# Performance work log

Measured on AMD Instinct MI355X. Metric: run time of the kernel, lower is better.

## Reference

```python
import jax, jax.numpy as jnp
import numpy as np

GRID_DIMS = (64, 64, 64)
GRID_LOWER = np.array([0.0, 0.0, 0.0], np.float32)
GRID_STEPS = np.array([0.015625, 0.015625, 0.015625], np.float32)
RADIUS = 0.03125
STENCIL = 2  # ceil(radius / step)


def _poly6(d2, h):
    # standard SPH poly6 smoothing kernel: 315/(64 pi h^9) (h^2 - d^2)^3, d <= h
    c = np.float32(315.0 / (64.0 * np.pi * h ** 9))
    return jnp.where(d2 <= h * h, c * (h * h - d2) ** 3, 0.0)


def particles2grid(locs, data, density):
    # locs [B,N,3], data [B,N,C], density [B,N] -> grid [B,X,Y,Z,C]
    B, N, _ = locs.shape
    C = data.shape[-1]
    X, Y, Z = GRID_DIMS
    dims = jnp.array(GRID_DIMS, jnp.int32)
    r = jnp.arange(-STENCIL, STENCIL + 1)
    offs = jnp.stack(jnp.meshgrid(r, r, r, indexing='ij'), -1).reshape(-1, 3)  # [K,3]
    base = jnp.floor((locs - GRID_LOWER) / GRID_STEPS).astype(jnp.int32)        # [B,N,3]
    cells = base[:, :, None, :] + offs                                          # [B,N,K,3]
    centers = GRID_LOWER + (cells.astype(locs.dtype) + 0.5) * GRID_STEPS
    d2 = jnp.sum((centers - locs[:, :, None, :]) ** 2, -1)                      # [B,N,K]
    w = _poly6(d2, RADIUS)
    w = jnp.where(jnp.all((cells >= 0) & (cells < dims), -1), w, 0.0)
    contrib = w[..., None] * (data / density[..., None])[:, :, None, :]         # [B,N,K,C]
    cells = jnp.clip(cells, 0, dims - 1)
    flat = (cells[..., 0] * Y + cells[..., 1]) * Z + cells[..., 2]              # [B,N,K]

    def splat(f, c):
        return jnp.zeros((X * Y * Z, C), data.dtype).at[f.reshape(-1)].add(c.reshape(-1, C))

    return jax.vmap(splat)(flat, contrib).reshape(B, X, Y, Z, C)


def grid2particles(grid, locs):
    # trilinear interpolation of grid [B,X,Y,Z,C] at particle locations [B,N,3]
    B, X, Y, Z, C = grid.shape
    dims = jnp.array([X, Y, Z], jnp.int32)
    pos = (locs - GRID_LOWER) / GRID_STEPS - 0.5                                # cell-center coords
    i0 = jnp.floor(pos).astype(jnp.int32)
    frac = pos - i0.astype(locs.dtype)
    gflat = grid.reshape(B, X * Y * Z, C)
    gather = jax.vmap(lambda g, f: g[f])                                        # [B,N] -> [B,N,C]
    out = jnp.zeros((B, locs.shape[1], C), grid.dtype)
    for dx in (0, 1):
        for dy in (0, 1):
            for dz in (0, 1):
                off = jnp.array([dx, dy, dz], jnp.int32)
                idx = i0 + off
                wd = jnp.where(off == 1, frac, 1.0 - frac)                      # [B,N,3]
                w = wd[..., 0] * wd[..., 1] * wd[..., 2]
                w = jnp.where(jnp.all((idx >= 0) & (idx < dims), -1), w, 0.0)
                idx = jnp.clip(idx, 0, dims - 1)
                flat = (idx[..., 0] * Y + idx[..., 1]) * Z + idx[..., 2]
                out = out + w[..., None] * gather(gflat, flat)
    return out


def conv3d(x, w, b):
    y = jax.lax.conv_general_dilated(x, w, (1, 1, 1), 'SAME',
                                     dimension_numbers=('NCDHW', 'OIDHW', 'NCDHW'))
    return y + b[None, :, None, None, None]


def prelu(x, a):
    return jnp.where(x >= 0, x, a * x)


def setup_inputs() -> dict:
    key = jax.random.key(0)
    ks = jax.random.split(key, 8)
    B, N = 2, 32768
    Cin, K, Cout = 4, 32, 4
    s = lambda fan: np.float32(1.0 / np.sqrt(fan * 27))
    return {
        'locs': jax.random.uniform(ks[0], (B, N, 3), jnp.float32),
        'data': jax.random.normal(ks[1], (B, N, Cin), jnp.float32),
        'density': jax.random.uniform(ks[2], (B, N), jnp.float32, 0.5, 1.5),
        'W0': jax.random.normal(ks[3], (K, Cin, 3, 3, 3), jnp.float32) * s(Cin),
        'b0': jnp.zeros((K,), jnp.float32),
        'W1': jax.random.normal(ks[4], (K, K, 3, 3, 3), jnp.float32) * s(K),
        'b1': jnp.zeros((K,), jnp.float32),
        'W2': jax.random.normal(ks[5], (K, K, 3, 3, 3), jnp.float32) * s(K),
        'b2': jnp.zeros((K,), jnp.float32),
        'W3': jax.random.normal(ks[6], (Cout, K, 3, 3, 3), jnp.float32) * s(K),
        'b3': jnp.zeros((Cout,), jnp.float32),
        'a0': jnp.full((1,), 0.25, jnp.float32),
        'a1': jnp.full((1,), 0.25, jnp.float32),
        'a2': jnp.full((1,), 0.25, jnp.float32),
    }


def reference(locs, data, density, W0, b0, W1, b1, W2, b2, W3, b3, a0, a1, a2):
    grid = particles2grid(locs, data, density)            # [B,X,Y,Z,Cin]
    g = jnp.transpose(grid, (0, 4, 1, 2, 3))              # NCDHW
    g = prelu(conv3d(g, W0, b0), a0)
    g = prelu(conv3d(g, W1, b1), a1)
    g = prelu(conv3d(g, W2, b2), a2)
    g = conv3d(g, W3, b3)
    g = jnp.transpose(g, (0, 2, 3, 4, 1))                 # [B,X,Y,Z,Cout]
    return grid2particles(g, locs)                        # [B,N,Cout]
```

## Files before the change

kernel.cpp:

```cpp
#include <hip/hip_runtime.h>

#define BATCH 2
#define NPART 32768
#define GD 64
#define NVOX (BATCH * GD * GD * GD)

typedef unsigned short ushortT;
typedef __attribute__((ext_vector_type(8))) short short8;
typedef __attribute__((ext_vector_type(16))) float float16;

__device__ __forceinline__ float poly6_c() {
    const double H9 = 1.0 / 35184372088832.0;
    return (float)(315.0 / (64.0 * 3.14159265358979323846 * H9));
}

__device__ __forceinline__ ushortT bf16_rne(float f) {
    unsigned int u = __float_as_uint(f);
    u = (u + 0x7fffu + ((u >> 16) & 1u)) >> 16;
    return (ushortT)u;
}

__device__ __forceinline__ int imax(int a, int b) { return a > b ? a : b; }
__device__ __forceinline__ int imin(int a, int b) { return a < b ? a : b; }

__device__ __forceinline__ void load_lds16(const void* g, void* l) {
    __builtin_amdgcn_global_load_lds(
        (const __attribute__((address_space(1))) void*)g,
        (__attribute__((address_space(3))) void*)l, 16, 0, 0);
}

__global__ void zero_ints_kernel(int* __restrict__ p, int n) {
    int t = blockIdx.x * blockDim.x + threadIdx.x;
    if (t < n) p[t] = 0;
}

__global__ __launch_bounds__(256) void bin_count_kernel(
    const float* __restrict__ locs, int* __restrict__ counts) {
    int t = blockIdx.x * blockDim.x + threadIdx.x;
    if (t >= BATCH * NPART) return;
    int b = t >> 15;
    int bx = ((int)floorf(locs[t * 3 + 0] * 64.0f)) >> 1;
    int by = ((int)floorf(locs[t * 3 + 1] * 64.0f)) >> 1;
    int bz = ((int)floorf(locs[t * 3 + 2] * 64.0f)) >> 1;
    atomicAdd(&counts[b * 32768 + ((bx * 32) + by) * 32 + bz], 1);
}

__global__ __launch_bounds__(256) void scanA_kernel(
    const int* __restrict__ counts, int* __restrict__ offsets,
    int* __restrict__ blockSum) {
    __shared__ int sh[256];
    int tid = threadIdx.x, g = blockIdx.x;
    int v = counts[g * 256 + tid];
    sh[tid] = v;
    __syncthreads();
    for (int off = 1; off < 256; off <<= 1) {
        int u = (tid >= off) ? sh[tid - off] : 0;
        __syncthreads();
        sh[tid] += u;
        __syncthreads();
    }
    offsets[g * 256 + tid] = sh[tid] - v;
    if (tid == 255) blockSum[g] = sh[255];
}

__global__ __launch_bounds__(256) void scanB_kernel(
    int* __restrict__ offsets, const int* __restrict__ blockSum) {
    __shared__ int sh[256];
    int tid = threadIdx.x, g = blockIdx.x;
    sh[tid] = (tid < g) ? blockSum[tid] : 0;
    __syncthreads();
    for (int off = 128; off > 0; off >>= 1) {
        if (tid < off) sh[tid] += sh[tid + off];
        __syncthreads();
    }
    offsets[g * 256 + tid] += sh[0];
    if (g == 255 && tid == 255) offsets[65536] = BATCH * NPART;
}

__global__ __launch_bounds__(256) void bin_scatter_kernel(
    const float* __restrict__ locs, const float* __restrict__ data,
    const float* __restrict__ density, const int* __restrict__ offsets,
    int* __restrict__ cursor, float* __restrict__ payload) {
    int t = blockIdx.x * blockDim.x + threadIdx.x;
    if (t >= BATCH * NPART) return;
    int b = t >> 15;
    float px = locs[t * 3 + 0];
    float py = locs[t * 3 + 1];
    float pz = locs[t * 3 + 2];
    int bx = ((int)floorf(px * 64.0f)) >> 1;
    int by = ((int)floorf(py * 64.0f)) >> 1;
    int bz = ((int)floorf(pz * 64.0f)) >> 1;
    int bb = b * 32768 + ((bx * 32) + by) * 32 + bz;
    int slot = atomicAdd(&cursor[bb], 1);
    int idx = offsets[bb] + slot;
    float inv_d = 1.0f / density[t];
    float4 p0 = {px, py, pz, data[t * 4 + 0] * inv_d};
    float4 p1 = {data[t * 4 + 1] * inv_d, data[t * 4 + 2] * inv_d,
                 data[t * 4 + 3] * inv_d, 0.f};
    *(float4*)(payload + idx * 8)     = p0;
    *(float4*)(payload + idx * 8 + 4) = p1;
}

__global__ __launch_bounds__(256) void splat_gather_kernel(
    const float* __restrict__ payload, const int* __restrict__ offsets,
    ushortT* __restrict__ g8) {
    __shared__ float plist[256 * 8];
    __shared__ int segS[36];
    __shared__ int segP[37];
    __shared__ int shTot[1];

    int wg = blockIdx.x;
    int sb = wg & 511, b = wg >> 9;
    int X0 = (sb >> 6) * 8, Y0 = ((sb >> 3) & 7) * 8, Z0 = (sb & 7) * 8;
    int tid = threadIdx.x;

    int bxlo = imax(0, (X0 - 2) >> 1), bxhi = imin(31, (X0 + 9) >> 1);
    int bylo = imax(0, (Y0 - 2) >> 1), byhi = imin(31, (Y0 + 9) >> 1);
    int bzlo = imax(0, (Z0 - 2) >> 1), bzhi = imin(31, (Z0 + 9) >> 1);
    int ny = byhi - bylo + 1;
    int ns = (bxhi - bxlo + 1) * ny;
    if (tid < ns) {
        int bx = bxlo + tid / ny, by = bylo + tid % ny;
        int row = b * 32768 + (bx * 32 + by) * 32;
        int s = offsets[row + bzlo];
        int e = offsets[row + bzhi + 1];
        segS[tid] = s;
        segP[tid] = e - s;
    }
    __syncthreads();
    if (tid == 0) {
        int p = 0;
        for (int k = 0; k < ns; ++k) { int len = segP[k]; segP[k] = p; p += len; }
        segP[ns] = p;
        shTot[0] = p;
    }
    __syncthreads();

    const float step = 0.015625f;
    const float h2 = 0.03125f * 0.03125f;
    const float cc = poly6_c();
    int total = shTot[0];

    int l = tid & 63, w = tid >> 6;
    int cx = X0 + 4 * (w >> 1) + (l >> 4);
    int cy = Y0 + 4 * (w & 1) + ((l >> 2) & 3);
    int cz0 = Z0 + (l & 3);
    float xc  = ((float)cx  + 0.5f) * step;
    float yc  = ((float)cy  + 0.5f) * step;
    float zc0 = ((float)cz0 + 0.5f) * step;
    float zc1 = zc0 + 4.0f * step;

    float a00 = 0.f, a01 = 0.f, a02 = 0.f, a03 = 0.f;
    float a10 = 0.f, a11 = 0.f, a12 = 0.f, a13 = 0.f;

    int nchunks = (total + 255) >> 8;
    for (int ch = 0; ch < nchunks; ++ch) {
        __syncthreads();
        int jj = (ch << 8) + tid;
        if (jj < total) {
            int k = 0;
            while (jj >= segP[k + 1]) ++k;
            int idx = segS[k] + (jj - segP[k]);
            *(float4*)(plist + tid * 8)     = *(const float4*)(payload + idx * 8);
            *(float4*)(plist + tid * 8 + 4) = *(const float4*)(payload + idx * 8 + 4);
        }
        __syncthreads();
        int cnt = imin(256, total - (ch << 8));
        for (int p = 0; p < cnt; ++p) {
            float4 pa = *(const float4*)(plist + p * 8);
            float dx = pa.x - xc, dy = pa.y - yc;
            float dxy2 = fmaf(dy, dy, dx * dx);
            if (!__any(dxy2 <= h2)) continue;
            float4 pv = *(const float4*)(plist + p * 8 + 4);
            float dz0 = pa.z - zc0;
            float d20 = fmaf(dz0, dz0, dxy2);
            float u0 = fmaxf(h2 - d20, 0.f);
            float w0 = (cc * u0) * (u0 * u0);
            a00 = fmaf(w0, pa.w, a00);
            a01 = fmaf(w0, pv.x, a01);
            a02 = fmaf(w0, pv.y, a02);
            a03 = fmaf(w0, pv.z, a03);
            float dz1 = pa.z - zc1;
            float d21 = fmaf(dz1, dz1, dxy2);
            float u1 = fmaxf(h2 - d21, 0.f);
            float w1 = (cc * u1) * (u1 * u1);
            a10 = fmaf(w1, pa.w, a10);
            a11 = fmaf(w1, pv.x, a11);
            a12 = fmaf(w1, pv.y, a12);
            a13 = fmaf(w1, pv.z, a13);
        }
    }

    size_t cellBase = (size_t)(((b * 64 + cx) * 64 + cy) * 64);
    short8 o;
    o[0] = (short)bf16_rne(a00); o[1] = (short)bf16_rne(a01);
    o[2] = (short)bf16_rne(a02); o[3] = (short)bf16_rne(a03);
    o[4] = 0; o[5] = 0; o[6] = 0; o[7] = 0;
    *(short8*)(g8 + (cellBase + cz0) * 8) = o;
    o[0] = (short)bf16_rne(a10); o[1] = (short)bf16_rne(a11);
    o[2] = (short)bf16_rne(a12); o[3] = (short)bf16_rne(a13);
    *(short8*)(g8 + (cellBase + cz0 + 4) * 8) = o;
}

__global__ void repack_all_kernel(
    const float* __restrict__ W0, const float* __restrict__ W1,
    const float* __restrict__ W2, const float* __restrict__ W3,
    short* __restrict__ Bp) {
    int t = blockIdx.x * blockDim.x + threadIdx.x;
    if (t >= 176 * 512) return;
    int kt = t >> 9;
    const float* W; int O, I, CINP, ktL;
    if (kt < 14)       { W = W0; O = 32; I = 4;  CINP = 8;  ktL = kt; }
    else if (kt < 68)  { W = W1; O = 32; I = 32; CINP = 32; ktL = kt - 14; }
    else if (kt < 122) { W = W2; O = 32; I = 32; CINP = 32; ktL = kt - 68; }
    else               { W = W3; O = 4;  I = 32; CINP = 32; ktL = kt - 122; }
    int l = (t >> 3) & 63, j = t & 7;
    int n = l & 31, q = l >> 5;
    int k = ktL * 16 + 8 * q + j;
    int tap = k / CINP;
    int ic  = k - tap * CINP;
    float v = 0.f;
    if (tap < 27 && ic < I && n < O) v = W[(n * I + ic) * 27 + tap];
    Bp[t] = (short)bf16_rne(v);
}

template <int ICG, int KT, bool FINAL>
__global__ __launch_bounds__(256, 3) void mfma_conv_kernel(
    const ushortT* __restrict__ in, const short* __restrict__ Bpack,
    const float* __restrict__ bias, const float* __restrict__ alpha,
    const float* __restrict__ zguard, void* __restrict__ outv) {
    constexpr int CIN = ICG * 8;
    constexpr int NCH = 24 * ICG * 34;
    __shared__ short lds[NCH * 8];
    int wg = ((blockIdx.x & 7) << 8) | (blockIdx.x >> 3);
    int zh = wg & 1, yq = (wg >> 1) & 15, xp = (wg >> 5) & 31, b = wg >> 10;
    int X0 = xp * 2, Y0 = yq * 4, Z0 = zh * 32;
    int tid = threadIdx.x;

    const ushortT* inb = in + (size_t)b * (64 * 64 * 64 * CIN);
#pragma unroll
    for (int it = 0; it < (NCH + 255) / 256; ++it) {
        int ccid = it * 256 + tid;
        if (ccid < NCH) {
            int col = ccid / (ICG * 34);
            int rem = ccid - col * (ICG * 34);
            int icg = rem / 34;
            int zi  = rem - icg * 34;
            int gx = X0 + col / 6 - 1;
            int gy = Y0 + col % 6 - 1;
            int gz = Z0 + zi - 1;
            const void* src = (const void*)zguard;
            if ((unsigned)gx < 64u && (unsigned)gy < 64u && (unsigned)gz < 64u)
                src = (const void*)(inb + ((size_t)(((gx * 64) + gy) * 64 + gz)) * CIN + icg * 8);
            load_lds16(src, (void*)(lds + ccid * 8));
        }
    }
    __syncthreads();

    int l = tid & 63, w = tid >> 6;
    int wx = w >> 1;
    int cyA = (w & 1) * 2, cyB = cyA + 1;
    int n = l & 31, q = l >> 5;

    float bval = FINAL ? (n < 4 ? bias[n] : 0.f) : bias[n];
    float16 accA, accB;
#pragma unroll
    for (int r = 0; r < 16; ++r) { accA[r] = bval; accB[r] = bval; }

    const short* bp = Bpack + (size_t)l * 8;
    int laneZ = (l & 31) * 8;

    short8 bf[4];
#pragma unroll
    for (int i = 0; i < 4; ++i) bf[i] = *(const short8*)(bp + i * 512);

#pragma unroll
    for (int kt = 0; kt < KT; ++kt) {
        short8 bcur = bf[kt & 3];
        if (kt + 4 < KT) bf[kt & 3] = *(const short8*)(bp + (kt + 4) * 512);
        int aofsA, aofsB;
        if constexpr (ICG == 1) {
            int tap0 = kt * 2, tap1 = kt * 2 + 1;
            if (tap1 > 26) tap1 = 26;
            int dx0 = tap0 / 9, r0 = tap0 - dx0 * 9, dy0 = r0 / 3, dz0 = r0 - dy0 * 3;
            int dx1 = tap1 / 9, r1 = tap1 - dx1 * 9, dy1 = r1 / 3, dz1 = r1 - dy1 * 3;
            int cA0 = (((wx + dx0) * 6 + (cyA + dy0)) * 34 + dz0) * 8;
            int cA1 = (((wx + dx1) * 6 + (cyA + dy1)) * 34 + dz1) * 8;
            int cB0 = (((wx + dx0) * 6 + (cyB + dy0)) * 34 + dz0) * 8;
            int cB1 = (((wx + dx1) * 6 + (cyB + dy1)) * 34 + dz1) * 8;
            aofsA = q ? cA1 : cA0;
            aofsB = q ? cB1 : cB0;
        } else {
            int tap = kt >> 1;
            int dx = tap / 9, rr = tap - dx * 9, dy = rr / 3, dz = rr - dy * 3;
            int icg = (kt & 1) * 2 + q;
            aofsA = ((((wx + dx) * 6 + (cyA + dy)) * ICG + icg) * 34 + dz) * 8;
            aofsB = ((((wx + dx) * 6 + (cyB + dy)) * ICG + icg) * 34 + dz) * 8;
        }
        short8 afragA = *(const short8*)(lds + aofsA + laneZ);
        short8 afragB = *(const short8*)(lds + aofsB + laneZ);
        accA = __builtin_amdgcn_mfma_f32_32x32x16_bf16(afragA, bcur, accA, 0, 0, 0);
        accB = __builtin_amdgcn_mfma_f32_32x32x16_bf16(afragB, bcur, accB, 0, 0, 0);
    }

    size_t baseA = (size_t)(((b * 64 + X0 + wx) * 64 + (Y0 + cyA)) * 64) + Z0;
    size_t baseB = (size_t)(((b * 64 + X0 + wx) * 64 + (Y0 + cyB)) * 64) + Z0;
    if (FINAL) {
        float* out = (float*)outv;
        if (n < 4) {
#pragma unroll
            for (int r = 0; r < 16; ++r) {
                int z = (r & 3) + 8 * (r >> 2) + 4 * q;
                out[(baseA + z) * 4 + n] = accA[r];
                out[(baseB + z) * 4 + n] = accB[r];
            }
        }
    } else {
        float a = alpha[0];
        ushortT* out = (ushortT*)outv;
#pragma unroll
        for (int r = 0; r < 16; ++r) {
            int z = (r & 3) + 8 * (r >> 2) + 4 * q;
            float vA = accA[r];
            vA = vA >= 0.f ? vA : a * vA;
            out[(baseA + z) * 32 + n] = bf16_rne(vA);
            float vB = accB[r];
            vB = vB >= 0.f ? vB : a * vB;
            out[(baseB + z) * 32 + n] = bf16_rne(vB);
        }
    }
}

__global__ __launch_bounds__(256) void gather_kernel(
    const float* __restrict__ grid, const float* __restrict__ locs,
    float* __restrict__ out) {
    int t = blockIdx.x * blockDim.x + threadIdx.x;
    if (t >= BATCH * NPART) return;
    int b = t >> 15;

    float px = locs[t * 3 + 0] * 64.0f - 0.5f;
    float py = locs[t * 3 + 1] * 64.0f - 0.5f;
    float pz = locs[t * 3 + 2] * 64.0f - 0.5f;
    int ix = (int)floorf(px);
    int iy = (int)floorf(py);
    int iz = (int)floorf(pz);
    float fx = px - (float)ix;
    float fy = py - (float)iy;
    float fz = pz - (float)iz;

    const float* gb = grid + (size_t)b * GD * GD * GD * 4;
    float o0 = 0.f, o1 = 0.f, o2 = 0.f, o3 = 0.f;

#pragma unroll
    for (int dx = 0; dx < 2; ++dx) {
        int x = ix + dx;
        if ((unsigned)x > 63u) continue;
        float wx = dx ? fx : 1.0f - fx;
#pragma unroll
        for (int dy = 0; dy < 2; ++dy) {
            int y = iy + dy;
            if ((unsigned)y > 63u) continue;
            float wy = dy ? fy : 1.0f - fy;
#pragma unroll
            for (int dz = 0; dz < 2; ++dz) {
                int z = iz + dz;
                if ((unsigned)z > 63u) continue;
                float wz = dz ? fz : 1.0f - fz;
                float w = wx * wy * wz;
                const float4 g = *(const float4*)(gb + (size_t)(((x * GD) + y) * GD + z) * 4);
                o0 += w * g.x; o1 += w * g.y; o2 += w * g.z; o3 += w * g.w;
            }
        }
    }
    out[t * 4 + 0] = o0;
    out[t * 4 + 1] = o1;
    out[t * 4 + 2] = o2;
    out[t * 4 + 3] = o3;
}

extern "C" void kernel_launch(void* const* d_in, const int* in_sizes, int n_in,
                              void* d_out, int out_size, void* d_ws, size_t ws_size,
                              hipStream_t stream) {
    const float* locs    = (const float*)d_in[0];
    const float* data    = (const float*)d_in[1];
    const float* density = (const float*)d_in[2];
    const float* W0 = (const float*)d_in[3];
    const float* b0 = (const float*)d_in[4];
    const float* W1 = (const float*)d_in[5];
    const float* b1 = (const float*)d_in[6];
    const float* W2 = (const float*)d_in[7];
    const float* b2 = (const float*)d_in[8];
    const float* W3 = (const float*)d_in[9];
    const float* b3 = (const float*)d_in[10];
    const float* a0 = (const float*)d_in[11];
    const float* a1 = (const float*)d_in[12];
    const float* a2 = (const float*)d_in[13];
    float* out = (float*)d_out;

    char* ws = (char*)d_ws;
    ushortT* g8  = (ushortT*)(ws);
    ushortT* gA  = (ushortT*)(ws + 8388608);
    ushortT* gB  = (ushortT*)(ws + 41943040);
    float*  gF   = (float*)(ws + 75497472);
    short*  Bp   = (short*)(ws + 83886080);
    short*  Bp0  = Bp;
    short*  Bp1  = Bp + 14 * 512;
    short*  Bp2  = Bp + 68 * 512;
    short*  Bp3  = Bp + 122 * 512;
    float* zguard   = (float*)(ws + 84066240);
    int*   counts   = (int*)(ws + 84066304);
    int*   cursor   = (int*)(ws + 84328448);
    int*   offsets  = (int*)(ws + 84590592);
    int*   blockSum = (int*)(ws + 84852752);
    float* payload  = (float*)(ws + 84853888);

    zero_ints_kernel<<<(131088 + 255) / 256, 256, 0, stream>>>((int*)zguard, 131088);
    bin_count_kernel<<<(BATCH * NPART) / 256, 256, 0, stream>>>(locs, counts);
    scanA_kernel<<<256, 256, 0, stream>>>(counts, offsets, blockSum);
    scanB_kernel<<<256, 256, 0, stream>>>(offsets, blockSum);
    bin_scatter_kernel<<<(BATCH * NPART) / 256, 256, 0, stream>>>(
        locs, data, density, offsets, cursor, payload);

    repack_all_kernel<<<(176 * 512 + 255) / 256, 256, 0, stream>>>(W0, W1, W2, W3, Bp);

    splat_gather_kernel<<<BATCH * 512, 256, 0, stream>>>(payload, offsets, g8);

    const int CGRID = 2048;
    mfma_conv_kernel< 1, 14, false><<<CGRID, 256, 0, stream>>>(g8, Bp0, b0, a0, zguard, gA);
    mfma_conv_kernel< 4, 54, false><<<CGRID, 256, 0, stream>>>(gA, Bp1, b1, a1, zguard, gB);
    mfma_conv_kernel< 4, 54, false><<<CGRID, 256, 0, stream>>>(gB, Bp2, b2, a2, zguard, gA);
    mfma_conv_kernel< 4, 54, true ><<<CGRID, 256, 0, stream>>>(gA, Bp3, b3, b3, zguard, gF);

    gather_kernel<<<(BATCH * NPART) / 256, 256, 0, stream>>>(gF, locs, out);
}
```

Before: 252.6 us.

## Split 32-channel conv input staging into two LDS phases to halve shared memory

For the 32-channel conv layers, the input halo tile is now staged into LDS in two channel-half phases instead of all at once. This halves the LDS footprint per workgroup so more workgroups can be resident. The weight repack is reordered to match, with input-channel half as the outer dimension and tap as the inner. The launch-bounds minimum-occupancy hint is dropped. The cost is an extra barrier and a second load phase that is not overlapped with compute.

```diff
diff --git a/kernel.cpp b/kernel.cpp
--- a/kernel.cpp
+++ b/kernel.cpp
@@ -209,53 +209,43 @@
     int t = blockIdx.x * blockDim.x + threadIdx.x;
     if (t >= 176 * 512) return;
     int kt = t >> 9;
-    const float* W; int O, I, CINP, ktL;
-    if (kt < 14)       { W = W0; O = 32; I = 4;  CINP = 8;  ktL = kt; }
-    else if (kt < 68)  { W = W1; O = 32; I = 32; CINP = 32; ktL = kt - 14; }
-    else if (kt < 122) { W = W2; O = 32; I = 32; CINP = 32; ktL = kt - 68; }
-    else               { W = W3; O = 4;  I = 32; CINP = 32; ktL = kt - 122; }
     int l = (t >> 3) & 63, j = t & 7;
     int n = l & 31, q = l >> 5;
-    int k = ktL * 16 + 8 * q + j;
-    int tap = k / CINP;
-    int ic  = k - tap * CINP;
     float v = 0.f;
-    if (tap < 27 && ic < I && n < O) v = W[(n * I + ic) * 27 + tap];
+    if (kt < 14) {
+        int k = kt * 16 + 8 * q + j;
+        int tap = k / 8, ic = k - tap * 8;
+        if (tap < 27 && ic < 4) v = W0[(n * 4 + ic) * 27 + tap];
+    } else {
+        int rem = kt - 14;
+        const float* W; int O;
+        if (rem < 54)       { W = W1; O = 32; }
+        else if (rem < 108) { W = W2; O = 32; rem -= 54; }
+        else                { W = W3; O = 4;  rem -= 108; }
+        int p = rem / 27, tap = rem - p * 27;
+        int ic = p * 16 + q * 8 + j;
+        if (n < O) v = W[(n * 32 + ic) * 27 + tap];
+    }
     Bp[t] = (short)bf16_rne(v);
 }
 
 template <int ICG, int KT, bool FINAL>
-__global__ __launch_bounds__(256, 3) void mfma_conv_kernel(
+__global__ __launch_bounds__(256) void mfma_conv_kernel(
     const ushortT* __restrict__ in, const short* __restrict__ Bpack,
     const float* __restrict__ bias, const float* __restrict__ alpha,
     const float* __restrict__ zguard, void* __restrict__ outv) {
     constexpr int CIN = ICG * 8;
-    constexpr int NCH = 24 * ICG * 34;
-    __shared__ short lds[NCH * 8];
+    constexpr int NPH  = (ICG == 4) ? 2 : 1;
+    constexpr int ICGH = (ICG == 4) ? 2 : 1;
+    constexpr int NCHH = 24 * ICGH * 34;
+    constexpr int KTH  = KT / NPH;
+    __shared__ short lds[NCHH * 8];
     int wg = ((blockIdx.x & 7) << 8) | (blockIdx.x >> 3);
     int zh = wg & 1, yq = (wg >> 1) & 15, xp = (wg >> 5) & 31, b = wg >> 10;
     int X0 = xp * 2, Y0 = yq * 4, Z0 = zh * 32;
     int tid = threadIdx.x;
 
     const ushortT* inb = in + (size_t)b * (64 * 64 * 64 * CIN);
-#pragma unroll
-    for (int it = 0; it < (NCH + 255) / 256; ++it) {
-        int ccid = it * 256 + tid;
-        if (ccid < NCH) {
-            int col = ccid / (ICG * 34);
-            int rem = ccid - col * (ICG * 34);
-            int icg = rem / 34;
-            int zi  = rem - icg * 34;
-            int gx = X0 + col / 6 - 1;
-            int gy = Y0 + col % 6 - 1;
-            int gz = Z0 + zi - 1;
-            const void* src = (const void*)zguard;
-            if ((unsigned)gx < 64u && (unsigned)gy < 64u && (unsigned)gz < 64u)
-                src = (const void*)(inb + ((size_t)(((gx * 64) + gy) * 64 + gz)) * CIN + icg * 8);
-            load_lds16(src, (void*)(lds + ccid * 8));
-        }
-    }
-    __syncthreads();
 
     int l = tid & 63, w = tid >> 6;
     int wx = w >> 1;
@@ -270,37 +260,60 @@
     const short* bp = Bpack + (size_t)l * 8;
     int laneZ = (l & 31) * 8;
 
-    short8 bf[4];
-#pragma unroll
-    for (int i = 0; i < 4; ++i) bf[i] = *(const short8*)(bp + i * 512);
-
-#pragma unroll
-    for (int kt = 0; kt < KT; ++kt) {
-        short8 bcur = bf[kt & 3];
-        if (kt + 4 < KT) bf[kt & 3] = *(const short8*)(bp + (kt + 4) * 512);
-        int aofsA, aofsB;
-        if constexpr (ICG == 1) {
-            int tap0 = kt * 2, tap1 = kt * 2 + 1;
-            if (tap1 > 26) tap1 = 26;
-            int dx0 = tap0 / 9, r0 = tap0 - dx0 * 9, dy0 = r0 / 3, dz0 = r0 - dy0 * 3;
-            int dx1 = tap1 / 9, r1 = tap1 - dx1 * 9, dy1 = r1 / 3, dz1 = r1 - dy1 * 3;
-            int cA0 = (((wx + dx0) * 6 + (cyA + dy0)) * 34 + dz0) * 8;
-            int cA1 = (((wx + dx1) * 6 + (cyA + dy1)) * 34 + dz1) * 8;
-            int cB0 = (((wx + dx0) * 6 + (cyB + dy0)) * 34 + dz0) * 8;
-            int cB1 = (((wx + dx1) * 6 + (cyB + dy1)) * 34 + dz1) * 8;
-            aofsA = q ? cA1 : cA0;
-            aofsB = q ? cB1 : cB0;
-        } else {
-            int tap = kt >> 1;
-            int dx = tap / 9, rr = tap - dx * 9, dy = rr / 3, dz = rr - dy * 3;
-            int icg = (kt & 1) * 2 + q;
-            aofsA = ((((wx + dx) * 6 + (cyA + dy)) * ICG + icg) * 34 + dz) * 8;
-            aofsB = ((((wx + dx) * 6 + (cyB + dy)) * ICG + icg) * 34 + dz) * 8;
-        }
-        short8 afragA = *(const short8*)(lds + aofsA + laneZ);
-        short8 afragB = *(const short8*)(lds + aofsB + laneZ);
-        accA = __builtin_amdgcn_mfma_f32_32x32x16_bf16(afragA, bcur, accA, 0, 0, 0);
-        accB = __builtin_amdgcn_mfma_f32_32x32x16_bf16(afragB, bcur, accB, 0, 0, 0);
+#pragma unroll
+    for (int p = 0; p < NPH; ++p) {
+        if (p) __syncthreads();
+#pragma unroll
+        for (int it = 0; it < (NCHH + 255) / 256; ++it) {
+            int ccid = it * 256 + tid;
+            if (ccid < NCHH) {
+                int col  = ccid / (ICGH * 34);
+                int rem  = ccid - col * (ICGH * 34);
+                int icgL = rem / 34;
+                int zi   = rem - icgL * 34;
+                int gx = X0 + col / 6 - 1;
+                int gy = Y0 + col % 6 - 1;
+                int gz = Z0 + zi - 1;
+                const void* src = (const void*)zguard;
+                if ((unsigned)gx < 64u && (unsigned)gy < 64u && (unsigned)gz < 64u)
+                    src = (const void*)(inb + ((size_t)(((gx * 64) + gy) * 64 + gz)) * CIN
+                                        + (p * ICGH + icgL) * 8);
+                load_lds16(src, (void*)(lds + ccid * 8));
+            }
+        }
+        __syncthreads();
+
+        const short* bph = bp + (size_t)(p * KTH) * 512;
+        short8 bf[4];
+#pragma unroll
+        for (int i = 0; i < 4; ++i) bf[i] = *(const short8*)(bph + i * 512);
+
+#pragma unroll
+        for (int t = 0; t < KTH; ++t) {
+            short8 bcur = bf[t & 3];
+            if (t + 4 < KTH) bf[t & 3] = *(const short8*)(bph + (t + 4) * 512);
+            int aofsA, aofsB;
+            if constexpr (ICG == 1) {
+                int tap0 = t * 2, tap1 = t * 2 + 1;
+                if (tap1 > 26) tap1 = 26;
+                int dx0 = tap0 / 9, r0 = tap0 - dx0 * 9, dy0 = r0 / 3, dz0 = r0 - dy0 * 3;
+                int dx1 = tap1 / 9, r1 = tap1 - dx1 * 9, dy1 = r1 / 3, dz1 = r1 - dy1 * 3;
+                int cA0 = (((wx + dx0) * 6 + (cyA + dy0)) * 34 + dz0) * 8;
+                int cA1 = (((wx + dx1) * 6 + (cyA + dy1)) * 34 + dz1) * 8;
+                int cB0 = (((wx + dx0) * 6 + (cyB + dy0)) * 34 + dz0) * 8;
+                int cB1 = (((wx + dx1) * 6 + (cyB + dy1)) * 34 + dz1) * 8;
+                aofsA = q ? cA1 : cA0;
+                aofsB = q ? cB1 : cB0;
+            } else {
+                int dx = t / 9, rr = t - dx * 9, dy = rr / 3, dz = rr - dy * 3;
+                aofsA = ((((wx + dx) * 6 + (cyA + dy)) * 2 + q) * 34 + dz) * 8;
+                aofsB = ((((wx + dx) * 6 + (cyB + dy)) * 2 + q) * 34 + dz) * 8;
+            }
+            short8 afragA = *(const short8*)(lds + aofsA + laneZ);
+            short8 afragB = *(const short8*)(lds + aofsB + laneZ);
+            accA = __builtin_amdgcn_mfma_f32_32x32x16_bf16(afragA, bcur, accA, 0, 0, 0);
+            accB = __builtin_amdgcn_mfma_f32_32x32x16_bf16(afragB, bcur, accB, 0, 0, 0);
+        }
     }
 
     size_t baseA = (size_t)(((b * 64 + X0 + wx) * 64 + (Y0 + cyA)) * 64) + Z0;
```

Measured after the change: 255.4 us. About the same (+1.1%).
